# Kernel optimization log

Hardware: AMD Instinct MI355X
Metric: run time of the kernel (lower is better)

Reference implementation:

```python
import jax, jax.numpy as jnp
import numpy as np

HIDDEN = 512
ENC = 512

def setup_inputs() -> dict:
    key = jax.random.key(0)
    k1, k2, k3, k4, k5 = jax.random.split(key, 5)
    decoder_hidden = jax.random.normal(k1, (256, HIDDEN), dtype=jnp.float32)
    encoder_outputs = jax.random.normal(k2, (256, 1024, ENC), dtype=jnp.float32)
    s = 1.0 / np.sqrt(HIDDEN)
    W_h = jax.random.uniform(k3, (HIDDEN, HIDDEN), minval=-s, maxval=s, dtype=jnp.float32)
    W_s = jax.random.uniform(k4, (HIDDEN, ENC), minval=-s, maxval=s, dtype=jnp.float32)
    v = jax.random.uniform(k5, (1, HIDDEN), minval=-s, maxval=s, dtype=jnp.float32)
    return {"decoder_hidden": decoder_hidden, "encoder_outputs": encoder_outputs,
            "W_h": W_h, "W_s": W_s, "v": v}

def reference(decoder_hidden, encoder_outputs, W_h, W_s, v):
    # proj_h: (b, hidden); proj_s: (b, l, hidden)
    proj_h = decoder_hidden @ W_h.T
    proj_s = jnp.einsum('ble,he->blh', encoder_outputs, W_s)
    # additive score: v^T tanh(W_h h + W_s s_i) -> (b, l)
    scores = jnp.einsum('blh,h->bl', jnp.tanh(proj_h[:, None, :] + proj_s), v[0])
    alpha = jax.nn.softmax(scores, axis=-1)
    context = jnp.einsum('bl,ble->be', alpha, encoder_outputs)
    return (context, alpha)
```

## Files before the change

kernel.cpp:

```cpp
#include <hip/hip_runtime.h>
#include <hip/hip_bf16.h>

#define HID 512
#define ENCD 512
#define NB 256
#define SEQ 1024
#define M_TOTAL (NB * SEQ)

typedef short bf16x8 __attribute__((ext_vector_type(8)));
typedef float floatx4 __attribute__((ext_vector_type(4)));

__device__ __forceinline__ unsigned short f2bf(float f) {
    unsigned u = __builtin_bit_cast(unsigned, f);
    u += 0x7FFFu + ((u >> 16) & 1u);
    return (unsigned short)(u >> 16);
}
__device__ __forceinline__ ushort4 cvt4(float4 a) {
    return make_ushort4(f2bf(a.x), f2bf(a.y), f2bf(a.z), f2bf(a.w));
}

__global__ __launch_bounds__(256) void prep_kernel(
    const float* __restrict__ dh,
    const float* __restrict__ W_h,
    const float* __restrict__ W_s,
    float* __restrict__ proj_h,
    unsigned short* __restrict__ Bshuf)
{
    __shared__ float sdh[2][HID];
    const int blk = blockIdx.x;
    const int t = threadIdx.x;
    const int b0 = blk * 2;

    ((float4*)&sdh[0][0])[t] = ((const float4*)(dh + (size_t)b0 * HID))[t];

    {
        const int id   = blk * 256 + t;
        const int lane = id & 63;
        const int nj   = (id >> 6) & 7;
        const int kt   = (id >> 9) & 15;
        const int wnG  = id >> 13;
        const int n = wnG * 128 + nj * 16 + (lane & 15);
        const int k = kt * 32 + (lane >> 4) * 8;
        const float* src = W_s + (size_t)n * HID + k;
        float4 s0 = *(const float4*)src;
        float4 s1 = *(const float4*)(src + 4);
        *(ushort4*)(Bshuf + (size_t)id * 8)     = cvt4(s0);
        *(ushort4*)(Bshuf + (size_t)id * 8 + 4) = cvt4(s1);
    }
    __syncthreads();

    #pragma unroll
    for (int i = 0; i < 2; ++i) {
        const int h = t + i * 256;
        const float4* wr = (const float4*)(W_h + (size_t)h * HID);
        float acc0 = 0.f, acc1 = 0.f;
        #pragma unroll 8
        for (int e4 = 0; e4 < HID / 4; ++e4) {
            float4 w  = wr[e4];
            float4 s0 = ((const float4*)&sdh[0][0])[e4];
            float4 s1 = ((const float4*)&sdh[1][0])[e4];
            acc0 += w.x * s0.x + w.y * s0.y + w.z * s0.z + w.w * s0.w;
            acc1 += w.x * s1.x + w.y * s1.y + w.z * s1.z + w.w * s1.w;
        }
        proj_h[(size_t)b0 * HID + h]       = acc0;
        proj_h[(size_t)(b0 + 1) * HID + h] = acc1;
    }
}

__global__ __launch_bounds__(512, 2) void score_gemm(
    const float* __restrict__ enc,
    const unsigned short* __restrict__ Bshuf,
    const float* __restrict__ proj_h,
    const float* __restrict__ v,
    float* __restrict__ scores)
{
    __shared__ unsigned short sA[2][128 * 40];
    __shared__ float sred[4][128];

    const int t    = threadIdx.x;
    const int wave = t >> 6;
    const int lane = t & 63;
    const int ln15 = lane & 15;
    const int lk   = lane >> 4;
    const int m0   = blockIdx.x * 128;
    const int bb   = m0 >> 10;
    const int wm   = (wave & 1) * 64;
    const int wnG  = wave >> 1;
    const int wn   = wnG * 128;

    floatx4 acc[4][8] = {};

    const int r0 = t >> 3, c4 = t & 7;
    const float* gA0 = enc + (size_t)(m0 + r0) * ENCD + c4 * 4;
    const float* gA1 = gA0 + (size_t)64 * ENCD;
    unsigned short* wp0 = &sA[0][r0 * 40 + c4 * 4];
    unsigned short* wp1 = &sA[0][(r0 + 64) * 40 + c4 * 4];
    const int bufStride = 128 * 40;

    const unsigned short* bbase = Bshuf + ((size_t)wnG * 8192 + lane) * 8;

    float4 p0a = *(const float4*)gA0;
    float4 p0b = *(const float4*)gA1;
    float4 qa  = *(const float4*)(gA0 + 32);
    float4 qb  = *(const float4*)(gA1 + 32);
    *(ushort4*)wp0 = cvt4(p0a);
    *(ushort4*)wp1 = cvt4(p0b);
    asm volatile("s_waitcnt lgkmcnt(0)" ::: "memory");
    __builtin_amdgcn_s_barrier();
    asm volatile("" ::: "memory");

    float4 ra = {}, rb = {};

    for (int kt = 0; kt < 16; kt += 2) {
        if (kt + 2 < 16) {
            ra = *(const float4*)(gA0 + (kt + 2) * 32);
            rb = *(const float4*)(gA1 + (kt + 2) * 32);
        }
        {
            bf16x8 bfrag[8];
            #pragma unroll
            for (int nj = 0; nj < 8; ++nj)
                bfrag[nj] = *(const bf16x8*)(bbase + (size_t)(kt * 8 + nj) * 512);
            bf16x8 afrag[4];
            #pragma unroll
            for (int mi = 0; mi < 4; ++mi)
                afrag[mi] = *(const bf16x8*)(&sA[0][(wm + mi * 16 + ln15) * 40 + lk * 8]);
            #pragma unroll
            for (int nj = 0; nj < 8; ++nj)
                #pragma unroll
                for (int mi = 0; mi < 4; ++mi)
                    acc[mi][nj] = __builtin_amdgcn_mfma_f32_16x16x32_bf16(
                        afrag[mi], bfrag[nj], acc[mi][nj], 0, 0, 0);
        }
        *(ushort4*)(wp0 + bufStride) = cvt4(qa);
        *(ushort4*)(wp1 + bufStride) = cvt4(qb);
        asm volatile("s_waitcnt lgkmcnt(0)" ::: "memory");
        __builtin_amdgcn_s_barrier();
        asm volatile("" ::: "memory");

        if (kt + 3 < 16) {
            qa = *(const float4*)(gA0 + (kt + 3) * 32);
            qb = *(const float4*)(gA1 + (kt + 3) * 32);
        }
        {
            bf16x8 bfrag[8];
            #pragma unroll
            for (int nj = 0; nj < 8; ++nj)
                bfrag[nj] = *(const bf16x8*)(bbase + (size_t)((kt + 1) * 8 + nj) * 512);
            bf16x8 afrag[4];
            #pragma unroll
            for (int mi = 0; mi < 4; ++mi)
                afrag[mi] = *(const bf16x8*)(&sA[1][(wm + mi * 16 + ln15) * 40 + lk * 8]);
            #pragma unroll
            for (int nj = 0; nj < 8; ++nj)
                #pragma unroll
                for (int mi = 0; mi < 4; ++mi)
                    acc[mi][nj] = __builtin_amdgcn_mfma_f32_16x16x32_bf16(
                        afrag[mi], bfrag[nj], acc[mi][nj], 0, 0, 0);
        }
        if (kt + 2 < 16) {
            *(ushort4*)wp0 = cvt4(ra);
            *(ushort4*)wp1 = cvt4(rb);
        }
        asm volatile("s_waitcnt lgkmcnt(0)" ::: "memory");
        __builtin_amdgcn_s_barrier();
        asm volatile("" ::: "memory");
    }

    float phv[8], vv[8];
    #pragma unroll
    for (int nj = 0; nj < 8; ++nj) {
        const int n = wn + nj * 16 + ln15;
        phv[nj] = proj_h[bb * HID + n];
        vv[nj]  = v[n];
    }

    #pragma unroll
    for (int mi = 0; mi < 4; ++mi) {
        #pragma unroll
        for (int r = 0; r < 4; ++r) {
            float s = 0.f;
            #pragma unroll
            for (int nj = 0; nj < 8; ++nj) {
                float x = acc[mi][nj][r] + phv[nj];
                float e = __expf(2.f * x);
                float th = 1.f - 2.f / (e + 1.f);
                s += vv[nj] * th;
            }
            s += __shfl_xor(s, 8, 64);
            s += __shfl_xor(s, 4, 64);
            s += __shfl_xor(s, 2, 64);
            s += __shfl_xor(s, 1, 64);
            if (ln15 == 0)
                sred[wnG][wm + mi * 16 + lk * 4 + r] = s;
        }
    }
    __syncthreads();
    if (t < 128)
        scores[m0 + t] = sred[0][t] + sred[1][t] + sred[2][t] + sred[3][t];
}

__global__ __launch_bounds__(1024) void softmax_ctx(
    const float* __restrict__ scores,
    const float* __restrict__ enc,
    float* __restrict__ ctx_out,
    float* __restrict__ alpha_out)
{
    __shared__ float salpha[SEQ];
    __shared__ float sctx[16][256];
    __shared__ float sbufA[16], sbufB[16];
    const int b    = blockIdx.x >> 1;
    const int half = blockIdx.x & 1;
    const int t = threadIdx.x;
    const int w = t >> 6;

    float sc = scores[(size_t)b * SEQ + t];

    float mx = sc;
    #pragma unroll
    for (int m = 32; m >= 1; m >>= 1) mx = fmaxf(mx, __shfl_xor(mx, m, 64));
    if ((t & 63) == 0) sbufA[w] = mx;
    __syncthreads();
    float gm = sbufA[0];
    #pragma unroll
    for (int i = 1; i < 16; ++i) gm = fmaxf(gm, sbufA[i]);

    float e0 = __expf(sc - gm);
    float ssum = e0;
    #pragma unroll
    for (int m = 32; m >= 1; m >>= 1) ssum += __shfl_xor(ssum, m, 64);
    if ((t & 63) == 0) sbufB[w] = ssum;
    __syncthreads();
    float tot = 0.f;
    #pragma unroll
    for (int i = 0; i < 16; ++i) tot += sbufB[i];
    const float inv = 1.f / tot;

    const float a0 = e0 * inv;
    salpha[t] = a0;
    if (half == 0) alpha_out[(size_t)b * SEQ + t] = a0;
    __syncthreads();

    const int tx = t & 63;
    const int ty = t >> 6;
    float4 acc = make_float4(0.f, 0.f, 0.f, 0.f);
    const float* ep = enc + (size_t)b * SEQ * ENCD + half * 256 + (size_t)tx * 4;
    #pragma unroll 8
    for (int l = ty; l < SEQ; l += 16) {
        float4 vv = *(const float4*)(ep + (size_t)l * ENCD);
        float a = salpha[l];
        acc.x += a * vv.x; acc.y += a * vv.y;
        acc.z += a * vv.z; acc.w += a * vv.w;
    }
    *(float4*)(&sctx[ty][tx * 4]) = acc;
    __syncthreads();

    if (t < 256) {
        float s = 0.f;
        #pragma unroll
        for (int y = 0; y < 16; ++y) s += sctx[y][t];
        ctx_out[(size_t)b * ENCD + half * 256 + t] = s;
    }
}

extern "C" void kernel_launch(void* const* d_in, const int* in_sizes, int n_in,
                              void* d_out, int out_size, void* d_ws, size_t ws_size,
                              hipStream_t stream) {
    const float* dh  = (const float*)d_in[0];
    const float* enc = (const float*)d_in[1];
    const float* W_h = (const float*)d_in[2];
    const float* W_s = (const float*)d_in[3];
    const float* v   = (const float*)d_in[4];

    float* ws = (float*)d_ws;
    float* proj_h = ws;
    float* scores = ws + 131072;
    unsigned short* Bshuf = (unsigned short*)(ws + 131072 + 262144);

    float* ctx   = (float*)d_out;
    float* alpha = (float*)d_out + NB * HID;

    prep_kernel<<<128, 256, 0, stream>>>(dh, W_h, W_s, proj_h, Bshuf);
    score_gemm<<<M_TOTAL / 128, 512, 0, stream>>>(enc, Bshuf, proj_h, v, scores);
    softmax_ctx<<<NB * 2, 1024, 0, stream>>>(scores, enc, ctx, alpha);
}
```

Before: 1.035 ms.

## Fuse score GEMM, online softmax and context into one per-batch kernel

Replaces the separate score GEMM and softmax/context kernels with a single kernel that uses one block per batch row. Each block walks the sequence in 64-row tiles: it stages each tile of encoder outputs in LDS as bf16, computes the tanh scores with MFMA, updates a running max and sum (online softmax), and accumulates the context from the same tile. The aim is to read the large encoder tensor from HBM once instead of twice and to drop the scores round trip and a launch. The cost is a grid of only 256 large blocks with heavy LDS use, so there is less parallelism to hide latency. The context pass also re-reads each tile in fp32 from global memory, which relies on cache hits.

```diff
diff --git a/kernel.cpp b/kernel.cpp
--- a/kernel.cpp
+++ b/kernel.cpp
@@ -5,10 +5,11 @@
 #define ENCD 512
 #define NB 256
 #define SEQ 1024
-#define M_TOTAL (NB * SEQ)
+#define LDSTR 520
 
 typedef short bf16x8 __attribute__((ext_vector_type(8)));
 typedef float floatx4 __attribute__((ext_vector_type(4)));
+typedef unsigned short ushort8v __attribute__((ext_vector_type(8)));
 
 __device__ __forceinline__ unsigned short f2bf(float f) {
     unsigned u = __builtin_bit_cast(unsigned, f);
@@ -17,6 +18,12 @@
 }
 __device__ __forceinline__ ushort4 cvt4(float4 a) {
     return make_ushort4(f2bf(a.x), f2bf(a.y), f2bf(a.z), f2bf(a.w));
+}
+__device__ __forceinline__ ushort8v cvt8(float4 a, float4 b) {
+    ushort8v r;
+    r[0]=f2bf(a.x); r[1]=f2bf(a.y); r[2]=f2bf(a.z); r[3]=f2bf(a.w);
+    r[4]=f2bf(b.x); r[5]=f2bf(b.y); r[6]=f2bf(b.z); r[7]=f2bf(b.w);
+    return r;
 }
 
 __global__ __launch_bounds__(256) void prep_kernel(
@@ -67,199 +74,197 @@
     }
 }
 
-__global__ __launch_bounds__(512, 2) void score_gemm(
+__global__ __launch_bounds__(512, 2) void fused_attn(
     const float* __restrict__ enc,
     const unsigned short* __restrict__ Bshuf,
     const float* __restrict__ proj_h,
     const float* __restrict__ v,
-    float* __restrict__ scores)
+    float* __restrict__ ctx_out,
+    float* __restrict__ alpha_out)
 {
-    __shared__ unsigned short sA[2][128 * 40];
-    __shared__ float sred[4][128];
+    __shared__ __align__(16) unsigned short sE[2][64 * LDSTR];
+    __shared__ float sred[8][64];
+    __shared__ float sscore[SEQ];
+    __shared__ float se[64];
+    __shared__ float sconst[4];
 
     const int t    = threadIdx.x;
-    const int wave = t >> 6;
+    const int w    = t >> 6;
     const int lane = t & 63;
     const int ln15 = lane & 15;
     const int lk   = lane >> 4;
-    const int m0   = blockIdx.x * 128;
-    const int bb   = m0 >> 10;
-    const int wm   = (wave & 1) * 64;
-    const int wnG  = wave >> 1;
-    const int wn   = wnG * 128;
-
-    floatx4 acc[4][8] = {};
-
-    const int r0 = t >> 3, c4 = t & 7;
-    const float* gA0 = enc + (size_t)(m0 + r0) * ENCD + c4 * 4;
-    const float* gA1 = gA0 + (size_t)64 * ENCD;
-    unsigned short* wp0 = &sA[0][r0 * 40 + c4 * 4];
-    unsigned short* wp1 = &sA[0][(r0 + 64) * 40 + c4 * 4];
-    const int bufStride = 128 * 40;
-
-    const unsigned short* bbase = Bshuf + ((size_t)wnG * 8192 + lane) * 8;
-
-    float4 p0a = *(const float4*)gA0;
-    float4 p0b = *(const float4*)gA1;
-    float4 qa  = *(const float4*)(gA0 + 32);
-    float4 qb  = *(const float4*)(gA1 + 32);
-    *(ushort4*)wp0 = cvt4(p0a);
-    *(ushort4*)wp1 = cvt4(p0b);
-    asm volatile("s_waitcnt lgkmcnt(0)" ::: "memory");
-    __builtin_amdgcn_s_barrier();
-    asm volatile("" ::: "memory");
-
-    float4 ra = {}, rb = {};
-
-    for (int kt = 0; kt < 16; kt += 2) {
-        if (kt + 2 < 16) {
-            ra = *(const float4*)(gA0 + (kt + 2) * 32);
-            rb = *(const float4*)(gA1 + (kt + 2) * 32);
-        }
-        {
-            bf16x8 bfrag[8];
-            #pragma unroll
-            for (int nj = 0; nj < 8; ++nj)
-                bfrag[nj] = *(const bf16x8*)(bbase + (size_t)(kt * 8 + nj) * 512);
-            bf16x8 afrag[4];
-            #pragma unroll
-            for (int mi = 0; mi < 4; ++mi)
-                afrag[mi] = *(const bf16x8*)(&sA[0][(wm + mi * 16 + ln15) * 40 + lk * 8]);
-            #pragma unroll
-            for (int nj = 0; nj < 8; ++nj)
+    const int b    = blockIdx.x;
+
+    if (t == 0) { sconst[0] = -3.0e38f; sconst[1] = 0.f; }
+
+    float phv[4], vv[4];
+    #pragma unroll
+    for (int nj = 0; nj < 4; ++nj) {
+        const int n = w * 64 + nj * 16 + ln15;
+        phv[nj] = proj_h[b * HID + n];
+        vv[nj]  = v[n];
+    }
+
+    const unsigned short* bb0 = Bshuf + ((size_t)(w >> 1) * 8192 + lane) * 8;
+    const int njo0 = (w & 1) * 4;
+
+    const float* encB = enc + (size_t)b * SEQ * ENCD;
+
+    {
+        const float* g = encB + (size_t)w * ENCD + lane * 8;
+        float4 f[16];
+        #pragma unroll
+        for (int p = 0; p < 8; ++p) {
+            f[2*p]   = *(const float4*)(g + (size_t)p * 8 * ENCD);
+            f[2*p+1] = *(const float4*)(g + (size_t)p * 8 * ENCD + 4);
+        }
+        #pragma unroll
+        for (int p = 0; p < 8; ++p)
+            *(ushort8v*)&sE[0][(p * 8 + w) * LDSTR + lane * 8] = cvt8(f[2*p], f[2*p+1]);
+    }
+    float C[8] = {0.f,0.f,0.f,0.f,0.f,0.f,0.f,0.f};
+    __syncthreads();
+
+    for (int ht = 0; ht < 16; ++ht) {
+        const int cur = ht & 1;
+        const unsigned short* sA = &sE[cur][0];
+        floatx4 acc[4][4] = {};
+
+        bf16x8 bfA[4], bfB[4];
+        #pragma unroll
+        for (int nj = 0; nj < 4; ++nj)
+            bfA[nj] = *(const bf16x8*)(bb0 + (size_t)(njo0 + nj) * 512);
+
+        float4 sf[16];
+
+        #pragma unroll
+        for (int kt2 = 0; kt2 < 8; ++kt2) {
+            const int kt = kt2 * 2;
+            #pragma unroll
+            for (int nj = 0; nj < 4; ++nj)
+                bfB[nj] = *(const bf16x8*)(bb0 + (size_t)((kt + 1) * 8 + njo0 + nj) * 512);
+            if (kt == 2 && ht < 15) {
+                const float* gn = encB + (size_t)((ht + 1) * 64 + w) * ENCD + lane * 8;
+                #pragma unroll
+                for (int p = 0; p < 8; ++p) {
+                    sf[2*p]   = *(const float4*)(gn + (size_t)p * 8 * ENCD);
+                    sf[2*p+1] = *(const float4*)(gn + (size_t)p * 8 * ENCD + 4);
+                }
+            }
+            {
+                bf16x8 af[4];
                 #pragma unroll
                 for (int mi = 0; mi < 4; ++mi)
-                    acc[mi][nj] = __builtin_amdgcn_mfma_f32_16x16x32_bf16(
-                        afrag[mi], bfrag[nj], acc[mi][nj], 0, 0, 0);
-        }
-        *(ushort4*)(wp0 + bufStride) = cvt4(qa);
-        *(ushort4*)(wp1 + bufStride) = cvt4(qb);
-        asm volatile("s_waitcnt lgkmcnt(0)" ::: "memory");
-        __builtin_amdgcn_s_barrier();
-        asm volatile("" ::: "memory");
-
-        if (kt + 3 < 16) {
-            qa = *(const float4*)(gA0 + (kt + 3) * 32);
-            qb = *(const float4*)(gA1 + (kt + 3) * 32);
-        }
-        {
-            bf16x8 bfrag[8];
-            #pragma unroll
-            for (int nj = 0; nj < 8; ++nj)
-                bfrag[nj] = *(const bf16x8*)(bbase + (size_t)((kt + 1) * 8 + nj) * 512);
-            bf16x8 afrag[4];
-            #pragma unroll
-            for (int mi = 0; mi < 4; ++mi)
-                afrag[mi] = *(const bf16x8*)(&sA[1][(wm + mi * 16 + ln15) * 40 + lk * 8]);
-            #pragma unroll
-            for (int nj = 0; nj < 8; ++nj)
+                    af[mi] = *(const bf16x8*)(&sA[(mi * 16 + ln15) * LDSTR + kt * 32 + lk * 8]);
+                #pragma unroll
+                for (int nj = 0; nj < 4; ++nj)
+                    #pragma unroll
+                    for (int mi = 0; mi < 4; ++mi)
+                        acc[mi][nj] = __builtin_amdgcn_mfma_f32_16x16x32_bf16(
+                            af[mi], bfA[nj], acc[mi][nj], 0, 0, 0);
+            }
+            if (kt + 2 < 16) {
+                #pragma unroll
+                for (int nj = 0; nj < 4; ++nj)
+                    bfA[nj] = *(const bf16x8*)(bb0 + (size_t)((kt + 2) * 8 + njo0 + nj) * 512);
+            }
+            {
+                bf16x8 af[4];
                 #pragma unroll
                 for (int mi = 0; mi < 4; ++mi)
-                    acc[mi][nj] = __builtin_amdgcn_mfma_f32_16x16x32_bf16(
-                        afrag[mi], bfrag[nj], acc[mi][nj], 0, 0, 0);
-        }
-        if (kt + 2 < 16) {
-            *(ushort4*)wp0 = cvt4(ra);
-            *(ushort4*)wp1 = cvt4(rb);
-        }
-        asm volatile("s_waitcnt lgkmcnt(0)" ::: "memory");
-        __builtin_amdgcn_s_barrier();
-        asm volatile("" ::: "memory");
-    }
-
-    float phv[8], vv[8];
-    #pragma unroll
-    for (int nj = 0; nj < 8; ++nj) {
-        const int n = wn + nj * 16 + ln15;
-        phv[nj] = proj_h[bb * HID + n];
-        vv[nj]  = v[n];
-    }
-
-    #pragma unroll
-    for (int mi = 0; mi < 4; ++mi) {
-        #pragma unroll
-        for (int r = 0; r < 4; ++r) {
-            float s = 0.f;
-            #pragma unroll
-            for (int nj = 0; nj < 8; ++nj) {
-                float x = acc[mi][nj][r] + phv[nj];
-                float e = __expf(2.f * x);
-                float th = 1.f - 2.f / (e + 1.f);
-                s += vv[nj] * th;
-            }
-            s += __shfl_xor(s, 8, 64);
-            s += __shfl_xor(s, 4, 64);
-            s += __shfl_xor(s, 2, 64);
-            s += __shfl_xor(s, 1, 64);
-            if (ln15 == 0)
-                sred[wnG][wm + mi * 16 + lk * 4 + r] = s;
-        }
+                    af[mi] = *(const bf16x8*)(&sA[(mi * 16 + ln15) * LDSTR + (kt + 1) * 32 + lk * 8]);
+                #pragma unroll
+                for (int nj = 0; nj < 4; ++nj)
+                    #pragma unroll
+                    for (int mi = 0; mi < 4; ++mi)
+                        acc[mi][nj] = __builtin_amdgcn_mfma_f32_16x16x32_bf16(
+                            af[mi], bfB[nj], acc[mi][nj], 0, 0, 0);
+            }
+        }
+
+        if (ht < 15) {
+            #pragma unroll
+            for (int p = 0; p < 8; ++p)
+                *(ushort8v*)&sE[1 - cur][(p * 8 + w) * LDSTR + lane * 8] = cvt8(sf[2*p], sf[2*p+1]);
+        }
+
+        #pragma unroll
+        for (int mi = 0; mi < 4; ++mi) {
+            #pragma unroll
+            for (int r = 0; r < 4; ++r) {
+                float s = 0.f;
+                #pragma unroll
+                for (int nj = 0; nj < 4; ++nj) {
+                    float x = acc[mi][nj][r] + phv[nj];
+                    float e = __expf(2.f * x);
+                    s += vv[nj] * (1.f - 2.f / (e + 1.f));
+                }
+                s += __shfl_xor(s, 8, 64);
+                s += __shfl_xor(s, 4, 64);
+                s += __shfl_xor(s, 2, 64);
+                s += __shfl_xor(s, 1, 64);
+                if (ln15 == 0) sred[w][mi * 16 + lk * 4 + r] = s;
+            }
+        }
+        __syncthreads();
+
+        if (w == 0) {
+            float sc = 0.f;
+            #pragma unroll
+            for (int g = 0; g < 8; ++g) sc += sred[g][lane];
+            sscore[ht * 64 + lane] = sc;
+            float mx = sc;
+            #pragma unroll
+            for (int m = 32; m >= 1; m >>= 1) mx = fmaxf(mx, __shfl_xor(mx, m, 64));
+            const float m_old = sconst[0];
+            const float m_new = fmaxf(m_old, mx);
+            const float rr    = __expf(m_old - m_new);
+            const float e     = __expf(sc - m_new);
+            se[lane] = e;
+            float es = e;
+            #pragma unroll
+            for (int m = 32; m >= 1; m >>= 1) es += __shfl_xor(es, m, 64);
+            if (lane == 0) {
+                sconst[0] = m_new;
+                sconst[1] = sconst[1] * rr + es;
+                sconst[2] = rr;
+            }
+        }
+        __syncthreads();
+
+        const float rr = sconst[2];
+        #pragma unroll
+        for (int j = 0; j < 8; ++j) C[j] *= rr;
+        const float* gc = encB + (size_t)(ht * 64 + w) * ENCD + lane * 8;
+        #pragma unroll
+        for (int i = 0; i < 8; ++i) {
+            const float ee = se[w + 8 * i];
+            float4 u0 = *(const float4*)(gc + (size_t)i * 8 * ENCD);
+            float4 u1 = *(const float4*)(gc + (size_t)i * 8 * ENCD + 4);
+            C[0] += ee * u0.x; C[1] += ee * u0.y; C[2] += ee * u0.z; C[3] += ee * u0.w;
+            C[4] += ee * u1.x; C[5] += ee * u1.y; C[6] += ee * u1.z; C[7] += ee * u1.w;
+        }
+    }
+
+    {
+        float* sctx = (float*)&sE[0][0];
+        *(float4*)&sctx[w * 512 + lane * 8]     = make_float4(C[0], C[1], C[2], C[3]);
+        *(float4*)&sctx[w * 512 + lane * 8 + 4] = make_float4(C[4], C[5], C[6], C[7]);
     }
     __syncthreads();
-    if (t < 128)
-        scores[m0 + t] = sred[0][t] + sred[1][t] + sred[2][t] + sred[3][t];
-}
-
-__global__ __launch_bounds__(1024) void softmax_ctx(
-    const float* __restrict__ scores,
-    const float* __restrict__ enc,
-    float* __restrict__ ctx_out,
-    float* __restrict__ alpha_out)
-{
-    __shared__ float salpha[SEQ];
-    __shared__ float sctx[16][256];
-    __shared__ float sbufA[16], sbufB[16];
-    const int b    = blockIdx.x >> 1;
-    const int half = blockIdx.x & 1;
-    const int t = threadIdx.x;
-    const int w = t >> 6;
-
-    float sc = scores[(size_t)b * SEQ + t];
-
-    float mx = sc;
-    #pragma unroll
-    for (int m = 32; m >= 1; m >>= 1) mx = fmaxf(mx, __shfl_xor(mx, m, 64));
-    if ((t & 63) == 0) sbufA[w] = mx;
-    __syncthreads();
-    float gm = sbufA[0];
-    #pragma unroll
-    for (int i = 1; i < 16; ++i) gm = fmaxf(gm, sbufA[i]);
-
-    float e0 = __expf(sc - gm);
-    float ssum = e0;
-    #pragma unroll
-    for (int m = 32; m >= 1; m >>= 1) ssum += __shfl_xor(ssum, m, 64);
-    if ((t & 63) == 0) sbufB[w] = ssum;
-    __syncthreads();
-    float tot = 0.f;
-    #pragma unroll
-    for (int i = 0; i < 16; ++i) tot += sbufB[i];
-    const float inv = 1.f / tot;
-
-    const float a0 = e0 * inv;
-    salpha[t] = a0;
-    if (half == 0) alpha_out[(size_t)b * SEQ + t] = a0;
-    __syncthreads();
-
-    const int tx = t & 63;
-    const int ty = t >> 6;
-    float4 acc = make_float4(0.f, 0.f, 0.f, 0.f);
-    const float* ep = enc + (size_t)b * SEQ * ENCD + half * 256 + (size_t)tx * 4;
-    #pragma unroll 8
-    for (int l = ty; l < SEQ; l += 16) {
-        float4 vv = *(const float4*)(ep + (size_t)l * ENCD);
-        float a = salpha[l];
-        acc.x += a * vv.x; acc.y += a * vv.y;
-        acc.z += a * vv.z; acc.w += a * vv.w;
-    }
-    *(float4*)(&sctx[ty][tx * 4]) = acc;
-    __syncthreads();
-
-    if (t < 256) {
-        float s = 0.f;
-        #pragma unroll
-        for (int y = 0; y < 16; ++y) s += sctx[y][t];
-        ctx_out[(size_t)b * ENCD + half * 256 + t] = s;
+    {
+        const float inv = 1.f / sconst[1];
+        const float m_f = sconst[0];
+        const float* sctx = (const float*)&sE[0][0];
+        float ssum = 0.f;
+        #pragma unroll
+        for (int g = 0; g < 8; ++g) ssum += sctx[g * 512 + t];
+        ctx_out[(size_t)b * HID + t] = ssum * inv;
+        #pragma unroll
+        for (int q = 0; q < 2; ++q) {
+            const int l = q * 512 + t;
+            alpha_out[(size_t)b * SEQ + l] = __expf(sscore[l] - m_f) * inv;
+        }
     }
 }
 
@@ -274,13 +279,11 @@
 
     float* ws = (float*)d_ws;
     float* proj_h = ws;
-    float* scores = ws + 131072;
-    unsigned short* Bshuf = (unsigned short*)(ws + 131072 + 262144);
+    unsigned short* Bshuf = (unsigned short*)(ws + 131072);
 
     float* ctx   = (float*)d_out;
     float* alpha = (float*)d_out + NB * HID;
 
     prep_kernel<<<128, 256, 0, stream>>>(dh, W_h, W_s, proj_h, Bshuf);
-    score_gemm<<<M_TOTAL / 128, 512, 0, stream>>>(enc, Bshuf, proj_h, v, scores);
-    softmax_ctx<<<NB * 2, 1024, 0, stream>>>(scores, enc, ctx, alpha);
-}
+    fused_attn<<<NB, 512, 0, stream>>>(enc, Bshuf, proj_h, v, ctx, alpha);
+}
```

After: 1.104 ms. 1.07x slower.
